# Kernel tuning notes

Measured on AMD Instinct MI355X. Metric: run time of the kernel, lower is better.

Reference implementation:

```python
import jax, jax.numpy as jnp
import numpy as np

D = 256   # hidden_dim
N = 1024  # total nodes
NP = 384  # paratope nodes
NE = 384  # epitope nodes
NC = 14   # atom channels


def setup_inputs() -> dict:
    key = jax.random.key(0)
    ks = jax.random.split(key, 24)
    s = 1.0 / np.sqrt(D)
    s3 = 1.0 / np.sqrt(3 * D)
    w = lambda k, shape, sc: (jax.random.normal(k, shape, jnp.float32) * sc)
    z = lambda: jnp.zeros((D,), jnp.float32)
    return {
        "H": w(ks[0], (N, D), 1.0),
        "X": w(ks[1], (N, NC, 3), 1.0),
        "paratope_mask": jnp.zeros((N,), bool).at[:NP].set(True),
        "epitope_mask": jnp.zeros((N,), bool).at[NP:NP + NE].set(True),
        "res_w1": w(ks[2], (1, D), 1.0), "res_b1": z(),
        "res_w2": w(ks[3], (D, D), s), "res_b2": z(),
        "atom_w1": w(ks[4], (1, D), 1.0), "atom_b1": z(),
        "atom_w2": w(ks[5], (D, D), s), "atom_b2": z(),
        "sim_weight": jnp.float32(0.5),
        "int_w1": w(ks[6], (3 * D, D), s3), "int_b1": z(),
        "int_w2": w(ks[7], (D, D), s), "int_b2": z(),
        "wl": w(ks[8], (D, D), s),
        "wr": w(ks[9], (D, D), s),
        "wg_w": w(ks[10], (D, D), s), "wg_b": z(),
        "wq_w": w(ks[11], (D, D), s), "wq_b": z(),
        "wk_w": w(ks[12], (D, D), s), "wk_b": z(),
        "wv_w": w(ks[13], (D, D), s), "wv_b": z(),
    }


def _mlp2(x, w1, b1, w2, b2):
    return jax.nn.silu(x @ w1 + b1) @ w2 + b2


def reference(H, X, paratope_mask, epitope_mask,
              res_w1, res_b1, res_w2, res_b2,
              atom_w1, atom_b1, atom_w2, atom_b2,
              sim_weight,
              int_w1, int_b1, int_w2, int_b2,
              wl, wr, wg_w, wg_b, wq_w, wq_b, wk_w, wk_b, wv_w, wv_b):
    p_idx = jnp.nonzero(paratope_mask, size=NP)[0]
    e_idx = jnp.nonzero(epitope_mask, size=NE)[0]
    Hp = H[p_idx]                      # [NP, D]
    He = H[e_idx]                      # [NE, D]
    Xp_ca = X[p_idx, 1]                # [NP, 3] (CA atom)
    Xe_ca = X[e_idx, 1]                # [NE, 3]

    dX = Xp_ca[:, None, :] - Xe_ca[None, :, :]         # [NP, NE, 3]
    S = jnp.sum(dX * dX, axis=-1, keepdims=True)       # [NP, NE, 1]
    # original computes S_residue and S_atom with identical formula
    S_res = _mlp2(S, res_w1, res_b1, res_w2, res_b2)
    S_atom = _mlp2(S, atom_w1, atom_b1, atom_w2, atom_b2)
    wmix = jax.nn.sigmoid(sim_weight)
    S_comb = wmix * S_res + (1.0 - wmix) * S_atom      # [NP, NE, D]

    Hp_e = jnp.broadcast_to(Hp[:, None, :], (NP, NE, D))
    He_e = jnp.broadcast_to(He[None, :, :], (NP, NE, D))
    Z_in = jnp.concatenate([Hp_e, He_e, S_comb], axis=-1)  # [NP, NE, 3D]
    Z = _mlp2(Z_in, int_w1, int_b1, int_w2, int_b2)        # [NP, NE, D]

    I = (Hp @ wl)[:, None, :] * (He @ wr)[None, :, :]      # outer-product interaction
    gate = jax.nn.sigmoid(Z @ wg_w + wg_b)
    f_tri = gate * I

    Q = Z @ wq_w + wq_b
    K = Z @ wk_w + wk_b
    V = Z @ wv_w + wv_b
    scores = jnp.einsum('ped,pfd->pef', Q, K) / (D ** 0.5)  # [NP, NE, NE]
    A = jax.nn.softmax(scores, axis=-1)
    f_att = jnp.einsum('pef,pfd->ped', A, V)

    H_tri = f_tri + f_att                                   # [NP, NE, D]
    return H.at[p_idx].set(H_tri.mean(axis=1))
```

## Files before the change

kernel.cpp:

```cpp
#include <hip/hip_runtime.h>

#define NPAR 384
#define NEPI 384
#define DD   256
#define NTAB 4096
#define SMAX 96.0f
#define SDELTA (SMAX / NTAB)
#define SINVD (NTAB / SMAX)

using bf16x8 = __bf16 __attribute__((ext_vector_type(8)));
using bf16x2 = __bf16 __attribute__((ext_vector_type(2)));
using f32x4  = float __attribute__((ext_vector_type(4)));

#if defined(__has_builtin)
#if __has_builtin(__builtin_amdgcn_cvt_pk_bf16_f32)
#define HAVE_PK_BF16 1
#endif
#endif

__device__ __forceinline__ float sigm(float x) { return 1.0f / (1.0f + __expf(-x)); }
__device__ __forceinline__ float silu(float x) { return x / (1.0f + __expf(-x)); }
__device__ __forceinline__ unsigned short f2bf(float f) {
  unsigned u = __float_as_uint(f);
  u += 0x7fffu + ((u >> 16) & 1u);
  return (unsigned short)(u >> 16);
}
__device__ __forceinline__ float bf2f(unsigned u16) {
  return __uint_as_float(u16 << 16);
}
__device__ __forceinline__ float bf2f_lo(unsigned w) {
  return __uint_as_float(w << 16);
}
__device__ __forceinline__ float bf2f_hi(unsigned w) {
  return __uint_as_float(w & 0xffff0000u);
}
__device__ __forceinline__ uint2 pack4(float a, float b, float c, float d) {
  uint2 r;
#ifdef HAVE_PK_BF16
  bf16x2 lo = __builtin_amdgcn_cvt_pk_bf16_f32(a, b);
  bf16x2 hi = __builtin_amdgcn_cvt_pk_bf16_f32(c, d);
  r.x = __builtin_bit_cast(unsigned, lo);
  r.y = __builtin_bit_cast(unsigned, hi);
#else
  r.x = (unsigned)f2bf(a) | ((unsigned)f2bf(b) << 16);
  r.y = (unsigned)f2bf(c) | ((unsigned)f2bf(d) << 16);
#endif
  return r;
}


__global__ void prep_kernel(
    const float* __restrict__ H, const float* __restrict__ wl,
    const float* __restrict__ wr, const float* __restrict__ int_w1,
    const float* __restrict__ res_w2, const float* __restrict__ atom_w2,
    const float* __restrict__ res_b2, const float* __restrict__ atom_b2,
    const float* __restrict__ int_b1, const float* __restrict__ simw,
    const float* __restrict__ wq_b, const float* __restrict__ wk_w,
    float* __restrict__ Hpl, float* __restrict__ Her,
    float* __restrict__ P1, float* __restrict__ P2,
    float* __restrict__ MrF, float* __restrict__ MaF,
    float* __restrict__ cvec, float* __restrict__ gv,
    float* __restrict__ wkT) {
  __shared__ float tile[32][33];
  const int b = blockIdx.x, t = threadIdx.x;
  if (b < 64) {
    const int bx = b & 7, by = b >> 3;
    const int tx = t & 31, ty = t >> 5;
    for (int r = 0; r < 32; r += 8)
      tile[ty + r][tx] = wk_w[(by * 32 + ty + r) * 256 + bx * 32 + tx];
    __syncthreads();
    for (int r = 0; r < 32; r += 8)
      wkT[(bx * 32 + ty + r) * 256 + by * 32 + tx] = tile[tx][ty + r];
  } else if (b < 576) {
    const int bb = b - 64;
    const int i = bb & 255;
    const bool isMa = bb >= 256;
    const float wmix = 1.0f / (1.0f + __expf(-simw[0]));
    const float sc = isMa ? (1.0f - wmix) : wmix;
    const float* W2 = isMa ? atom_w2 : res_w2;
    float acc = 0.f;
#pragma unroll 8
    for (int k = 0; k < 256; ++k)
      acc += W2[i * 256 + k] * int_w1[(512 + k) * 256 + t];
    (isMa ? MaF : MrF)[i * 256 + t] = acc * sc;
  } else if (b < 584) {
    const int bb = b - 576;
    const float wmix = 1.0f / (1.0f + __expf(-simw[0]));
    float acc = (bb == 0) ? int_b1[t] : 0.f;
#pragma unroll
    for (int k = bb * 32; k < bb * 32 + 32; ++k) {
      float bm = wmix * res_b2[k] + (1.0f - wmix) * atom_b2[k];
      acc += bm * int_w1[(512 + k) * 256 + t];
    }
    atomicAdd(&cvec[t], acc);
  } else if (b < 648) {
    const int lane = t & 63, w = t >> 6;
    const int d = (b - 584) * 4 + w;
    float acc = 0.f;
#pragma unroll
    for (int i = 0; i < 4; ++i) {
      const int c = i * 64 + lane;
      acc += wk_w[d * 256 + c] * wq_b[c];
    }
    acc += __shfl_xor(acc, 1);
    acc += __shfl_xor(acc, 2);
    acc += __shfl_xor(acc, 4);
    acc += __shfl_xor(acc, 8);
    acc += __shfl_xor(acc, 16);
    acc += __shfl_xor(acc, 32);
    if (lane == 0) gv[d] = acc;
  } else {
    const int idx = b - 648;
    const int seg = idx / 384, r = idx % 384;
    const float* A;
    const float* B;
    float* C;
    switch (seg) {
      case 0:  A = H + r * 256;            B = wl;              C = Hpl + r * 256; break;
      case 1:  A = H + (NPAR + r) * 256;   B = wr;              C = Her + r * 256; break;
      case 2:  A = H + r * 256;            B = int_w1;          C = P1 + r * 256;  break;
      default: A = H + (NPAR + r) * 256;   B = int_w1 + 65536;  C = P2 + r * 256;  break;
    }
    float acc = 0.f;
#pragma unroll 8
    for (int k = 0; k < 256; ++k)
      acc += A[k] * B[k * 256 + t];
    C[t] = acc;
  }
}

__global__ void mm_rows(const float* __restrict__ A, const float* __restrict__ B,
                        float* __restrict__ C) {
  const int r = blockIdx.x, j = threadIdx.x;
  float acc = 0.f;
#pragma unroll 8
  for (int k = 0; k < 256; ++k)
    acc += A[r * 256 + k] * B[k * 256 + j];
  C[r * 256 + j] = acc;
}

__global__ void pack_kernel(const float* __restrict__ MrF, const float* __restrict__ MaF,
                            const float* __restrict__ w2, const float* __restrict__ wg,
                            const float* __restrict__ WqkF, unsigned short* __restrict__ wpack) {
  const int idx = blockIdx.x * 256 + threadIdx.x;
  const int m = idx >> 16;
  const int r = idx & 65535;
  const int chunk = r >> 9;
  const int lane = (r >> 3) & 63;
  const int j = r & 7;
  const int k = (chunk >> 4) * 32 + (lane >> 4) * 8 + j;
  const int n = (chunk & 15) * 16 + (lane & 15);
  const float* src;
  switch (m) {
    case 0: src = MrF; break;
    case 1: src = MaF; break;
    case 2: src = w2; break;
    case 3: src = wg; break;
    default: src = WqkF; break;
  }
  wpack[idx] = f2bf(src[k * 256 + n]);
}


__device__ __forceinline__ void zero_acc4(f32x4 (&acc)[4][4]) {
#pragma unroll
  for (int mt = 0; mt < 4; ++mt)
#pragma unroll
    for (int nt = 0; nt < 4; ++nt)
      acc[mt][nt] = (f32x4){0.f, 0.f, 0.f, 0.f};
}

__device__ __forceinline__ void gemm4(f32x4 (&acc)[4][4],
                                      const unsigned short* __restrict__ wp,
                                      const unsigned short* ub, int lane, int wv) {
  const int l15 = lane & 15, l4 = lane >> 4;
#pragma unroll
  for (int ks = 0; ks < 8; ++ks) {
    bf16x8 a[4];
#pragma unroll
    for (int mt = 0; mt < 4; ++mt)
      a[mt] = *reinterpret_cast<const bf16x8*>(wp + ((ks * 16 + wv * 4 + mt) * 64 + lane) * 8);
#pragma unroll
    for (int nt = 0; nt < 4; ++nt) {
      bf16x8 b = *reinterpret_cast<const bf16x8*>(ub + (nt * 16 + l15) * 264 + ks * 32 + l4 * 8);
#pragma unroll
      for (int mt = 0; mt < 4; ++mt)
        acc[mt][nt] = __builtin_amdgcn_mfma_f32_16x16x32_bf16(a[mt], b, acc[mt][nt], 0, 0, 0);
    }
  }
}

__device__ __forceinline__ void fill_u(unsigned short* ub, const float* Sv,
                                       const float* __restrict__ w1,
                                       const float* __restrict__ b1, int t) {
  const int dg = t & 31, rb = t >> 5;
  const f32x4 w1a = *reinterpret_cast<const f32x4*>(&w1[dg * 8]);
  const f32x4 w1b = *reinterpret_cast<const f32x4*>(&w1[dg * 8 + 4]);
  const f32x4 b1a = *reinterpret_cast<const f32x4*>(&b1[dg * 8]);
  const f32x4 b1b = *reinterpret_cast<const f32x4*>(&b1[dg * 8 + 4]);
#pragma unroll
  for (int i = 0; i < 8; ++i) {
    const int e = rb + i * 8;
    const float s = Sv[e];
    uint2 lo = pack4(silu(fmaf(s, w1a[0], b1a[0])), silu(fmaf(s, w1a[1], b1a[1])),
                     silu(fmaf(s, w1a[2], b1a[2])), silu(fmaf(s, w1a[3], b1a[3])));
    uint2 hi = pack4(silu(fmaf(s, w1b[0], b1b[0])), silu(fmaf(s, w1b[1], b1b[1])),
                     silu(fmaf(s, w1b[2], b1b[2])), silu(fmaf(s, w1b[3], b1b[3])));
    uint4 pk = {lo.x, lo.y, hi.x, hi.y};
    *reinterpret_cast<uint4*>(&ub[e * 264 + dg * 8]) = pk;
  }
}


__global__ __launch_bounds__(256, 3) void tab_kernel(
    const float* __restrict__ res_w1, const float* __restrict__ res_b1,
    const float* __restrict__ atom_w1, const float* __restrict__ atom_b1,
    const unsigned short* __restrict__ wpack, unsigned short* __restrict__ tab) {
  __shared__ __align__(16) unsigned short ubuf[64 * 264];
  __shared__ float Sv[64];
  const int t = threadIdx.x, lane = t & 63, wv = t >> 6;
  const int l15 = lane & 15, l4 = lane >> 4;
  const int n0 = blockIdx.x * 64;
  if (t < 64) Sv[t] = (n0 + t) * SDELTA;
  __syncthreads();
  f32x4 acc[4][4];
  zero_acc4(acc);
  fill_u(ubuf, Sv, res_w1, res_b1, t);
  __syncthreads();
  gemm4(acc, wpack + 0 * 65536, ubuf, lane, wv);
  __syncthreads();
  fill_u(ubuf, Sv, atom_w1, atom_b1, t);
  __syncthreads();
  gemm4(acc, wpack + 1 * 65536, ubuf, lane, wv);
#pragma unroll
  for (int mt = 0; mt < 4; ++mt) {
    const int d = wv * 64 + mt * 16 + l4 * 4;
#pragma unroll
    for (int nt = 0; nt < 4; ++nt) {
      const int n = n0 + nt * 16 + l15;
      *reinterpret_cast<uint2*>(&tab[n * 256 + d]) =
          pack4(acc[mt][nt][0], acc[mt][nt][1], acc[mt][nt][2], acc[mt][nt][3]);
    }
  }
}


__global__ __launch_bounds__(256, 3) void pair_kernel(
    const float* __restrict__ Xg, const unsigned short* __restrict__ tab,
    const float* __restrict__ int_b2, const float* __restrict__ wg_b,
    const unsigned short* __restrict__ wpack, const float* __restrict__ cvec,
    const float* __restrict__ P1, const float* __restrict__ P2,
    const float* __restrict__ Hpl, const float* __restrict__ Her,
    float* __restrict__ ftri, unsigned short* __restrict__ Zsw) {
  __shared__ __align__(16) unsigned short ubuf[64 * 264];
  __shared__ float Sv[64];
  __shared__ float pc[DD];
  const int t = threadIdx.x, lane = t & 63, wv = t >> 6;
  const int l15 = lane & 15, l4 = lane >> 4;
  const int p = blockIdx.x / 6, cc = blockIdx.x % 6, e0 = cc * 64;
  const int d0 = wv * 64;

  if (t < 64) {
    const int e = e0 + t;
    float dx = Xg[p * 42 + 3] - Xg[(NPAR + e) * 42 + 3];
    float dy = Xg[p * 42 + 4] - Xg[(NPAR + e) * 42 + 4];
    float dz = Xg[p * 42 + 5] - Xg[(NPAR + e) * 42 + 5];
    Sv[t] = dx * dx + dy * dy + dz * dz;
  }
  pc[t] = P1[p * DD + t] + cvec[t];
  __syncthreads();

  {
    const int dg = t & 31, rb = t >> 5;
    const f32x4 pca = *reinterpret_cast<const f32x4*>(&pc[dg * 8]);
    const f32x4 pcb = *reinterpret_cast<const f32x4*>(&pc[dg * 8 + 4]);
#pragma unroll
    for (int i = 0; i < 8; ++i) {
      const int e = rb + i * 8;
      float sv = Sv[e] * SINVD;
      int idx = (int)sv;
      idx = idx > (NTAB - 2) ? (NTAB - 2) : idx;
      const float fr = sv - (float)idx;
      const uint4 t0 = *reinterpret_cast<const uint4*>(&tab[idx * 256 + dg * 8]);
      const uint4 t1 = *reinterpret_cast<const uint4*>(&tab[(idx + 1) * 256 + dg * 8]);
      const f32x4 p2a = *reinterpret_cast<const f32x4*>(&P2[(e0 + e) * DD + dg * 8]);
      const f32x4 p2b = *reinterpret_cast<const f32x4*>(&P2[(e0 + e) * DD + dg * 8 + 4]);
      float z0 = bf2f_lo(t0.x), z1 = bf2f_hi(t0.x), z2 = bf2f_lo(t0.y), z3 = bf2f_hi(t0.y);
      float z4 = bf2f_lo(t0.z), z5 = bf2f_hi(t0.z), z6 = bf2f_lo(t0.w), z7 = bf2f_hi(t0.w);
      z0 = fmaf(fr, bf2f_lo(t1.x) - z0, z0) + pca[0] + p2a[0];
      z1 = fmaf(fr, bf2f_hi(t1.x) - z1, z1) + pca[1] + p2a[1];
      z2 = fmaf(fr, bf2f_lo(t1.y) - z2, z2) + pca[2] + p2a[2];
      z3 = fmaf(fr, bf2f_hi(t1.y) - z3, z3) + pca[3] + p2a[3];
      z4 = fmaf(fr, bf2f_lo(t1.z) - z4, z4) + pcb[0] + p2b[0];
      z5 = fmaf(fr, bf2f_hi(t1.z) - z5, z5) + pcb[1] + p2b[1];
      z6 = fmaf(fr, bf2f_lo(t1.w) - z6, z6) + pcb[2] + p2b[2];
      z7 = fmaf(fr, bf2f_hi(t1.w) - z7, z7) + pcb[3] + p2b[3];
      uint2 lo = pack4(silu(z0), silu(z1), silu(z2), silu(z3));
      uint2 hi = pack4(silu(z4), silu(z5), silu(z6), silu(z7));
      uint4 pk = {lo.x, lo.y, hi.x, hi.y};
      *reinterpret_cast<uint4*>(&ubuf[e * 264 + dg * 8]) = pk;
    }
  }
  __syncthreads();

  f32x4 acc[4][4];
  zero_acc4(acc);
  gemm4(acc, wpack + 2 * 65536, ubuf, lane, wv);
  __syncthreads();
#pragma unroll
  for (int mt = 0; mt < 4; ++mt) {
    const int d = d0 + mt * 16 + l4 * 4;
    const f32x4 bb = *reinterpret_cast<const f32x4*>(&int_b2[d]);
#pragma unroll
    for (int nt = 0; nt < 4; ++nt) {
      const int e = nt * 16 + l15;
      *reinterpret_cast<uint2*>(&ubuf[e * 264 + d]) =
          pack4(acc[mt][nt][0] + bb[0], acc[mt][nt][1] + bb[1],
                acc[mt][nt][2] + bb[2], acc[mt][nt][3] + bb[3]);
    }
  }
  __syncthreads();

  {
    unsigned short* Zd = Zsw + (size_t)p * 98304 + (size_t)(cc * 4 + wv) * 4096 + lane * 8;
#pragma unroll
    for (int ks = 0; ks < 8; ++ks) {
      *reinterpret_cast<uint4*>(Zd + ks * 512) =
          *reinterpret_cast<const uint4*>(&ubuf[(wv * 16 + l15) * 264 + ks * 32 + l4 * 8]);
    }
  }

  zero_acc4(acc);
  gemm4(acc, wpack + 3 * 65536, ubuf, lane, wv);
#pragma unroll
  for (int mt = 0; mt < 4; ++mt) {
    const int d = d0 + mt * 16 + l4 * 4;
    const f32x4 bb = *reinterpret_cast<const f32x4*>(&wg_b[d]);
    const f32x4 hl = *reinterpret_cast<const f32x4*>(&Hpl[p * DD + d]);
    f32x4 fs = (f32x4){0.f, 0.f, 0.f, 0.f};
#pragma unroll
    for (int nt = 0; nt < 4; ++nt) {
      const int e = e0 + nt * 16 + l15;
      const f32x4 hr = *reinterpret_cast<const f32x4*>(&Her[e * DD + d]);
#pragma unroll
      for (int r = 0; r < 4; ++r)
        fs[r] += sigm(acc[mt][nt][r] + bb[r]) * hr[r];
    }
#pragma unroll
    for (int r = 0; r < 4; ++r) {
      float v = fs[r] * hl[r];
      v += __shfl_xor(v, 1);
      v += __shfl_xor(v, 2);
      v += __shfl_xor(v, 4);
      v += __shfl_xor(v, 8);
      if (l15 == 0) atomicAdd(&ftri[p * DD + d + r], v);
    }
  }
}


__global__ __launch_bounds__(256, 3) void attn_kernel(
    const unsigned short* __restrict__ Zsw, const float* __restrict__ gv,
    const unsigned short* __restrict__ wpack, float* __restrict__ cbufg) {
  __shared__ __align__(16) unsigned short Tc[64 * 264];
  __shared__ float red[256];
  __shared__ float red2[256];
  const int t = threadIdx.x, lane = t & 63, wv = t >> 6;
  const int l15 = lane & 15, l4 = lane >> 4;
  const int xcd = blockIdx.x & 7, inner = blockIdx.x >> 3;
  const int p = (inner / 6) * 8 + xcd, c = inner % 6;
  const unsigned short* Zsp = Zsw + (size_t)p * 98304;
  const unsigned short* wqk = wpack + 4 * 65536;

  {
    f32x4 ta[4][4];
    zero_acc4(ta);
    const unsigned short* Tb = Zsp + (size_t)(c * 4) * 4096 + lane * 8;
    bf16x8 bcur[4], bnxt[4];
#pragma unroll
    for (int nt = 0; nt < 4; ++nt)
      bcur[nt] = *reinterpret_cast<const bf16x8*>(Tb + nt * 4096);
#pragma unroll
    for (int ks = 0; ks < 8; ++ks) {
      if (ks < 7) {
#pragma unroll
        for (int nt = 0; nt < 4; ++nt)
          bnxt[nt] = *reinterpret_cast<const bf16x8*>(Tb + nt * 4096 + (ks + 1) * 512);
      }
      bf16x8 a[4];
#pragma unroll
      for (int mt = 0; mt < 4; ++mt)
        a[mt] = *reinterpret_cast<const bf16x8*>(wqk + ((ks * 16 + wv * 4 + mt) * 64 + lane) * 8);
#pragma unroll
      for (int nt = 0; nt < 4; ++nt)
#pragma unroll
        for (int mt = 0; mt < 4; ++mt)
          ta[mt][nt] = __builtin_amdgcn_mfma_f32_16x16x32_bf16(a[mt], bcur[nt], ta[mt][nt], 0, 0, 0);
      if (ks < 7) {
#pragma unroll
        for (int nt = 0; nt < 4; ++nt) bcur[nt] = bnxt[nt];
      }
    }
#pragma unroll
    for (int mt = 0; mt < 4; ++mt) {
      const int d = wv * 64 + mt * 16 + l4 * 4;
      const f32x4 gq = *reinterpret_cast<const f32x4*>(&gv[d]);
#pragma unroll
      for (int nt = 0; nt < 4; ++nt) {
        const int e = nt * 16 + l15;
        *reinterpret_cast<uint2*>(&Tc[e * 264 + d]) =
            pack4((ta[mt][nt][0] + gq[0]) * 0.0625f, (ta[mt][nt][1] + gq[1]) * 0.0625f,
                  (ta[mt][nt][2] + gq[2]) * 0.0625f, (ta[mt][nt][3] + gq[3]) * 0.0625f);
      }
    }
  }
  __syncthreads();

  f32x4 sc[4][6];
#pragma unroll
  for (int mt = 0; mt < 4; ++mt)
#pragma unroll
    for (int s = 0; s < 6; ++s) sc[mt][s] = (f32x4){0.f, 0.f, 0.f, 0.f};

  {
    const unsigned short* Sb = Zsp + (size_t)wv * 4096 + lane * 8;
    bf16x8 bcur[6], bnxt[6];
#pragma unroll
    for (int s = 0; s < 6; ++s)
      bcur[s] = *reinterpret_cast<const bf16x8*>(Sb + s * 16384);
#pragma unroll
    for (int ks = 0; ks < 8; ++ks) {
      if (ks < 7) {
#pragma unroll
        for (int s = 0; s < 6; ++s)
          bnxt[s] = *reinterpret_cast<const bf16x8*>(Sb + s * 16384 + (ks + 1) * 512);
      }
      bf16x8 a[4];
#pragma unroll
      for (int mt = 0; mt < 4; ++mt)
        a[mt] = *reinterpret_cast<const bf16x8*>(&Tc[(mt * 16 + l15) * 264 + ks * 32 + l4 * 8]);
#pragma unroll
      for (int s = 0; s < 6; ++s)
#pragma unroll
        for (int mt = 0; mt < 4; ++mt)
          sc[mt][s] = __builtin_amdgcn_mfma_f32_16x16x32_bf16(a[mt], bcur[s], sc[mt][s], 0, 0, 0);
      if (ks < 7) {
#pragma unroll
        for (int s = 0; s < 6; ++s) bcur[s] = bnxt[s];
      }
    }
  }

  float rmax[4][4];
#pragma unroll
  for (int mt = 0; mt < 4; ++mt) {
#pragma unroll
    for (int r = 0; r < 4; ++r) {
      float m = -1e30f;
#pragma unroll
      for (int s = 0; s < 6; ++s) m = fmaxf(m, sc[mt][s][r]);
      m = fmaxf(m, __shfl_xor(m, 1));
      m = fmaxf(m, __shfl_xor(m, 2));
      m = fmaxf(m, __shfl_xor(m, 4));
      m = fmaxf(m, __shfl_xor(m, 8));
      rmax[mt][r] = m;
    }
  }
  if (l15 == 0) {
#pragma unroll
    for (int mt = 0; mt < 4; ++mt)
#pragma unroll
      for (int r = 0; r < 4; ++r)
        red[wv * 64 + mt * 16 + l4 * 4 + r] = rmax[mt][r];
  }
  __syncthreads();
#pragma unroll
  for (int mt = 0; mt < 4; ++mt) {
#pragma unroll
    for (int r = 0; r < 4; ++r) {
      const int row = mt * 16 + l4 * 4 + r;
      rmax[mt][r] = fmaxf(fmaxf(red[row], red[64 + row]), fmaxf(red[128 + row], red[192 + row]));
    }
  }

  float rsum[4][4];
#pragma unroll
  for (int mt = 0; mt < 4; ++mt) {
#pragma unroll
    for (int r = 0; r < 4; ++r) {
      float sSum = 0.f;
#pragma unroll
      for (int s = 0; s < 6; ++s) {
        float e = __expf(sc[mt][s][r] - rmax[mt][r]);
        sc[mt][s][r] = e;
        sSum += e;
      }
      sSum += __shfl_xor(sSum, 1);
      sSum += __shfl_xor(sSum, 2);
      sSum += __shfl_xor(sSum, 4);
      sSum += __shfl_xor(sSum, 8);
      rsum[mt][r] = sSum;
    }
  }
  if (l15 == 0) {
#pragma unroll
    for (int mt = 0; mt < 4; ++mt)
#pragma unroll
      for (int r = 0; r < 4; ++r)
        red2[wv * 64 + mt * 16 + l4 * 4 + r] = rsum[mt][r];
  }
  __syncthreads();
  float rinv[4][4];
#pragma unroll
  for (int mt = 0; mt < 4; ++mt) {
#pragma unroll
    for (int r = 0; r < 4; ++r) {
      const int row = mt * 16 + l4 * 4 + r;
      rinv[mt][r] = 1.0f / (red2[row] + red2[64 + row] + red2[128 + row] + red2[192 + row]);
    }
  }

#pragma unroll
  for (int s = 0; s < 6; ++s) {
    float v = 0.f;
#pragma unroll
    for (int mt = 0; mt < 4; ++mt)
#pragma unroll
      for (int r = 0; r < 4; ++r)
        v += sc[mt][s][r] * rinv[mt][r];
    v += __shfl_xor(v, 16);
    v += __shfl_xor(v, 32);
    if (lane < 16)
      atomicAdd(&cbufg[p * NEPI + s * 64 + wv * 16 + lane], v);
  }
}


__global__ __launch_bounds__(256) void out_kernel(
    const unsigned short* __restrict__ Zsw, const float* __restrict__ ftri,
    const float* __restrict__ cbufg, const float* __restrict__ wvw,
    const float* __restrict__ wvb, float* __restrict__ out) {
  __shared__ float cb[NEPI];
  __shared__ float part[16][257];
  __shared__ float u[DD];
  const int p = blockIdx.x, t = threadIdx.x;
  const int lane = t & 63, wv = t >> 6;
  const int l15 = lane & 15, l4 = lane >> 4;
  for (int i = t; i < NEPI; i += 256) cb[i] = cbufg[p * NEPI + i];
  __syncthreads();
  const unsigned short* Zsp = Zsw + (size_t)p * 98304;
  float a16[16];
#pragma unroll
  for (int j = 0; j < 16; ++j) a16[j] = 0.f;
#pragma unroll 4
  for (int grp = 0; grp < 24; ++grp) {
    const float w = cb[grp * 16 + l15];
    const uint4 z0 = *reinterpret_cast<const uint4*>(Zsp + grp * 4096 + wv * 512 + lane * 8);
    const uint4 z1 = *reinterpret_cast<const uint4*>(Zsp + grp * 4096 + (wv + 4) * 512 + lane * 8);
    a16[0] = fmaf(w, bf2f(z0.x & 0xffffu), a16[0]);
    a16[1] = fmaf(w, bf2f(z0.x >> 16), a16[1]);
    a16[2] = fmaf(w, bf2f(z0.y & 0xffffu), a16[2]);
    a16[3] = fmaf(w, bf2f(z0.y >> 16), a16[3]);
    a16[4] = fmaf(w, bf2f(z0.z & 0xffffu), a16[4]);
    a16[5] = fmaf(w, bf2f(z0.z >> 16), a16[5]);
    a16[6] = fmaf(w, bf2f(z0.w & 0xffffu), a16[6]);
    a16[7] = fmaf(w, bf2f(z0.w >> 16), a16[7]);
    a16[8]  = fmaf(w, bf2f(z1.x & 0xffffu), a16[8]);
    a16[9]  = fmaf(w, bf2f(z1.x >> 16), a16[9]);
    a16[10] = fmaf(w, bf2f(z1.y & 0xffffu), a16[10]);
    a16[11] = fmaf(w, bf2f(z1.y >> 16), a16[11]);
    a16[12] = fmaf(w, bf2f(z1.z & 0xffffu), a16[12]);
    a16[13] = fmaf(w, bf2f(z1.z >> 16), a16[13]);
    a16[14] = fmaf(w, bf2f(z1.w & 0xffffu), a16[14]);
    a16[15] = fmaf(w, bf2f(z1.w >> 16), a16[15]);
  }
#pragma unroll
  for (int j = 0; j < 8; ++j) part[l15][wv * 32 + l4 * 8 + j] = a16[j];
#pragma unroll
  for (int j = 0; j < 8; ++j) part[l15][128 + wv * 32 + l4 * 8 + j] = a16[8 + j];
  __syncthreads();
  float uu = 0.f;
#pragma unroll
  for (int g = 0; g < 16; ++g) uu += part[g][t];
  u[t] = uu;
  __syncthreads();
  float acc = ftri[p * DD + t] + 384.0f * wvb[t];
#pragma unroll 8
  for (int d = 0; d < DD; ++d)
    acc = fmaf(u[d], wvw[d * DD + t], acc);
  out[p * DD + t] = acc * (1.0f / 384.0f);
}


extern "C" void kernel_launch(void* const* d_in, const int* in_sizes, int n_in,
                              void* d_out, int out_size, void* d_ws, size_t ws_size,
                              hipStream_t stream) {
  (void)in_sizes; (void)n_in; (void)out_size; (void)ws_size;
  const float* H = (const float*)d_in[0];
  const float* X = (const float*)d_in[1];
  const float* res_w1 = (const float*)d_in[4];
  const float* res_b1 = (const float*)d_in[5];
  const float* res_w2 = (const float*)d_in[6];
  const float* res_b2 = (const float*)d_in[7];
  const float* atom_w1 = (const float*)d_in[8];
  const float* atom_b1 = (const float*)d_in[9];
  const float* atom_w2 = (const float*)d_in[10];
  const float* atom_b2 = (const float*)d_in[11];
  const float* simw = (const float*)d_in[12];
  const float* int_w1 = (const float*)d_in[13];
  const float* int_b1 = (const float*)d_in[14];
  const float* int_w2 = (const float*)d_in[15];
  const float* int_b2 = (const float*)d_in[16];
  const float* wl = (const float*)d_in[17];
  const float* wr = (const float*)d_in[18];
  const float* wg_w = (const float*)d_in[19];
  const float* wg_b = (const float*)d_in[20];
  const float* wq_w = (const float*)d_in[21];
  const float* wq_b = (const float*)d_in[22];
  const float* wk_w = (const float*)d_in[23];
  const float* wv_w = (const float*)d_in[25];
  const float* wv_b = (const float*)d_in[26];

  char* ws = (char*)d_ws;
  unsigned short* wpack = (unsigned short*)(ws + 0);
  float* MrF   = (float*)(ws + 655360);
  float* MaF   = (float*)(ws + 917504);
  float* WqkF  = (float*)(ws + 1179648);
  float* wkT   = (float*)(ws + 1441792);
  float* cvec  = (float*)(ws + 1703936);
  float* gv    = (float*)(ws + 1704960);
  float* P1    = (float*)(ws + 1705984);
  float* P2    = (float*)(ws + 2099200);
  float* Hpl   = (float*)(ws + 2492416);
  float* Her   = (float*)(ws + 2885632);
  float* ftri  = (float*)(ws + 3278848);
  float* cbufg = (float*)(ws + 3672064);
  unsigned short* Zsw = (unsigned short*)(ws + 4261888);
  unsigned short* tab = (unsigned short*)(ws + 79759360);

  hipMemsetAsync(ftri, 0, 393216 + 589824, stream);
  hipMemsetAsync(cvec, 0, DD * sizeof(float), stream);
  prep_kernel<<<2184, 256, 0, stream>>>(H, wl, wr, int_w1, res_w2, atom_w2,
                                        res_b2, atom_b2, int_b1, simw, wq_b, wk_w,
                                        Hpl, Her, P1, P2, MrF, MaF, cvec, gv, wkT);
  mm_rows<<<256, 256, 0, stream>>>(wq_w, wkT, WqkF);
  pack_kernel<<<1280, 256, 0, stream>>>(MrF, MaF, int_w2, wg_w, WqkF, wpack);
  tab_kernel<<<NTAB / 64, 256, 0, stream>>>(res_w1, res_b1, atom_w1, atom_b1, wpack, tab);
  pair_kernel<<<2304, 256, 0, stream>>>(X, tab, int_b2, wg_b, wpack, cvec,
                                        P1, P2, Hpl, Her, ftri, Zsw);
  attn_kernel<<<2304, 256, 0, stream>>>(Zsw, gv, wpack, cbufg);
  out_kernel<<<384, 256, 0, stream>>>(Zsw, ftri, cbufg, wv_w, wv_b, (float*)d_out);
  hipMemcpyAsync((float*)d_out + NPAR * DD, H + NPAR * DD,
                 (1024 - NPAR) * DD * sizeof(float), hipMemcpyDeviceToDevice, stream);
}
```

Measured before the change: 344.5 us.

## Fold Wq·WkT into prep kernel and split output reduction across more blocks

The separate wk transpose and mm_rows launch are removed. The Wq·Wk^T product is now computed inside prep_kernel by reading wk rows directly with vector loads. The cvec bias reduction becomes a single block, which drops one memset and the atomics. The output kernel is split into outa_kernel, which spreads each paratope's weighted Z reduction over three blocks and combines them with atomics into ubufg, and out2_kernel, which applies wv; this raises parallelism over the 75MB Z read at the cost of one extra launch.

Measured after the change: 343.2 us. Within noise of the previous version (-0.4%).

```diff
diff --git a/kernel.cpp b/kernel.cpp
--- a/kernel.cpp
+++ b/kernel.cpp
@@ -56,25 +56,17 @@
     const float* __restrict__ res_b2, const float* __restrict__ atom_b2,
     const float* __restrict__ int_b1, const float* __restrict__ simw,
     const float* __restrict__ wq_b, const float* __restrict__ wk_w,
+    const float* __restrict__ wq_w,
     float* __restrict__ Hpl, float* __restrict__ Her,
     float* __restrict__ P1, float* __restrict__ P2,
     float* __restrict__ MrF, float* __restrict__ MaF,
     float* __restrict__ cvec, float* __restrict__ gv,
-    float* __restrict__ wkT) {
-  __shared__ float tile[32][33];
+    float* __restrict__ WqkF) {
+  __shared__ float sbuf[256];
   const int b = blockIdx.x, t = threadIdx.x;
-  if (b < 64) {
-    const int bx = b & 7, by = b >> 3;
-    const int tx = t & 31, ty = t >> 5;
-    for (int r = 0; r < 32; r += 8)
-      tile[ty + r][tx] = wk_w[(by * 32 + ty + r) * 256 + bx * 32 + tx];
-    __syncthreads();
-    for (int r = 0; r < 32; r += 8)
-      wkT[(bx * 32 + ty + r) * 256 + by * 32 + tx] = tile[tx][ty + r];
-  } else if (b < 576) {
-    const int bb = b - 64;
-    const int i = bb & 255;
-    const bool isMa = bb >= 256;
+  if (b < 512) {
+    const int i = b & 255;
+    const bool isMa = b >= 256;
     const float wmix = 1.0f / (1.0f + __expf(-simw[0]));
     const float sc = isMa ? (1.0f - wmix) : wmix;
     const float* W2 = isMa ? atom_w2 : res_w2;
@@ -83,19 +75,18 @@
     for (int k = 0; k < 256; ++k)
       acc += W2[i * 256 + k] * int_w1[(512 + k) * 256 + t];
     (isMa ? MaF : MrF)[i * 256 + t] = acc * sc;
-  } else if (b < 584) {
-    const int bb = b - 576;
+  } else if (b == 512) {
     const float wmix = 1.0f / (1.0f + __expf(-simw[0]));
-    float acc = (bb == 0) ? int_b1[t] : 0.f;
-#pragma unroll
-    for (int k = bb * 32; k < bb * 32 + 32; ++k) {
+    float acc = int_b1[t];
+#pragma unroll 8
+    for (int k = 0; k < 256; ++k) {
       float bm = wmix * res_b2[k] + (1.0f - wmix) * atom_b2[k];
       acc += bm * int_w1[(512 + k) * 256 + t];
     }
-    atomicAdd(&cvec[t], acc);
-  } else if (b < 648) {
+    cvec[t] = acc;
+  } else if (b < 577) {
     const int lane = t & 63, w = t >> 6;
-    const int d = (b - 584) * 4 + w;
+    const int d = (b - 513) * 4 + w;
     float acc = 0.f;
 #pragma unroll
     for (int i = 0; i < 4; ++i) {
@@ -109,8 +100,23 @@
     acc += __shfl_xor(acc, 16);
     acc += __shfl_xor(acc, 32);
     if (lane == 0) gv[d] = acc;
+  } else if (b < 833) {
+    const int r = b - 577;
+    sbuf[t] = wq_w[r * 256 + t];
+    __syncthreads();
+    const float* wkrow = wk_w + t * 256;
+    float a0 = 0.f, a1 = 0.f, a2 = 0.f, a3 = 0.f;
+#pragma unroll 4
+    for (int k = 0; k < 256; k += 4) {
+      const f32x4 wv4 = *reinterpret_cast<const f32x4*>(&wkrow[k]);
+      a0 = fmaf(sbuf[k + 0], wv4[0], a0);
+      a1 = fmaf(sbuf[k + 1], wv4[1], a1);
+      a2 = fmaf(sbuf[k + 2], wv4[2], a2);
+      a3 = fmaf(sbuf[k + 3], wv4[3], a3);
+    }
+    WqkF[r * 256 + t] = (a0 + a1) + (a2 + a3);
   } else {
-    const int idx = b - 648;
+    const int idx = b - 833;
     const int seg = idx / 384, r = idx % 384;
     const float* A;
     const float* B;
@@ -127,16 +133,6 @@
       acc += A[k] * B[k * 256 + t];
     C[t] = acc;
   }
-}
-
-__global__ void mm_rows(const float* __restrict__ A, const float* __restrict__ B,
-                        float* __restrict__ C) {
-  const int r = blockIdx.x, j = threadIdx.x;
-  float acc = 0.f;
-#pragma unroll 8
-  for (int k = 0; k < 256; ++k)
-    acc += A[r * 256 + k] * B[k * 256 + j];
-  C[r * 256 + j] = acc;
 }
 
 __global__ void pack_kernel(const float* __restrict__ MrF, const float* __restrict__ MaF,
@@ -536,25 +532,25 @@
 }
 
 
-__global__ __launch_bounds__(256) void out_kernel(
-    const unsigned short* __restrict__ Zsw, const float* __restrict__ ftri,
-    const float* __restrict__ cbufg, const float* __restrict__ wvw,
-    const float* __restrict__ wvb, float* __restrict__ out) {
-  __shared__ float cb[NEPI];
+__global__ __launch_bounds__(256) void outa_kernel(
+    const unsigned short* __restrict__ Zsw, const float* __restrict__ cbufg,
+    float* __restrict__ ubufg) {
+  __shared__ float cb[128];
   __shared__ float part[16][257];
-  __shared__ float u[DD];
-  const int p = blockIdx.x, t = threadIdx.x;
+  const int p = blockIdx.x / 3, th = blockIdx.x % 3, g0 = th * 8;
+  const int t = threadIdx.x;
   const int lane = t & 63, wv = t >> 6;
   const int l15 = lane & 15, l4 = lane >> 4;
-  for (int i = t; i < NEPI; i += 256) cb[i] = cbufg[p * NEPI + i];
+  if (t < 128) cb[t] = cbufg[p * NEPI + g0 * 16 + t];
   __syncthreads();
   const unsigned short* Zsp = Zsw + (size_t)p * 98304;
   float a16[16];
 #pragma unroll
   for (int j = 0; j < 16; ++j) a16[j] = 0.f;
-#pragma unroll 4
-  for (int grp = 0; grp < 24; ++grp) {
-    const float w = cb[grp * 16 + l15];
+#pragma unroll
+  for (int gr = 0; gr < 8; ++gr) {
+    const int grp = g0 + gr;
+    const float w = cb[gr * 16 + l15];
     const uint4 z0 = *reinterpret_cast<const uint4*>(Zsp + grp * 4096 + wv * 512 + lane * 8);
     const uint4 z1 = *reinterpret_cast<const uint4*>(Zsp + grp * 4096 + (wv + 4) * 512 + lane * 8);
     a16[0] = fmaf(w, bf2f(z0.x & 0xffffu), a16[0]);
@@ -582,7 +578,17 @@
   float uu = 0.f;
 #pragma unroll
   for (int g = 0; g < 16; ++g) uu += part[g][t];
-  u[t] = uu;
+  atomicAdd(&ubufg[p * DD + t], uu);
+}
+
+
+__global__ __launch_bounds__(256) void out2_kernel(
+    const float* __restrict__ ubufg, const float* __restrict__ ftri,
+    const float* __restrict__ wvw, const float* __restrict__ wvb,
+    float* __restrict__ out) {
+  __shared__ float u[DD];
+  const int p = blockIdx.x, t = threadIdx.x;
+  u[t] = ubufg[p * DD + t];
   __syncthreads();
   float acc = ftri[p * DD + t] + 384.0f * wvb[t];
 #pragma unroll 8
@@ -626,30 +632,29 @@
   float* MrF   = (float*)(ws + 655360);
   float* MaF   = (float*)(ws + 917504);
   float* WqkF  = (float*)(ws + 1179648);
-  float* wkT   = (float*)(ws + 1441792);
-  float* cvec  = (float*)(ws + 1703936);
-  float* gv    = (float*)(ws + 1704960);
-  float* P1    = (float*)(ws + 1705984);
-  float* P2    = (float*)(ws + 2099200);
-  float* Hpl   = (float*)(ws + 2492416);
-  float* Her   = (float*)(ws + 2885632);
-  float* ftri  = (float*)(ws + 3278848);
-  float* cbufg = (float*)(ws + 3672064);
-  unsigned short* Zsw = (unsigned short*)(ws + 4261888);
-  unsigned short* tab = (unsigned short*)(ws + 79759360);
-
-  hipMemsetAsync(ftri, 0, 393216 + 589824, stream);
-  hipMemsetAsync(cvec, 0, DD * sizeof(float), stream);
-  prep_kernel<<<2184, 256, 0, stream>>>(H, wl, wr, int_w1, res_w2, atom_w2,
-                                        res_b2, atom_b2, int_b1, simw, wq_b, wk_w,
-                                        Hpl, Her, P1, P2, MrF, MaF, cvec, gv, wkT);
-  mm_rows<<<256, 256, 0, stream>>>(wq_w, wkT, WqkF);
+  float* cvec  = (float*)(ws + 1441792);
+  float* gv    = (float*)(ws + 1442816);
+  float* P1    = (float*)(ws + 1443840);
+  float* P2    = (float*)(ws + 1837056);
+  float* Hpl   = (float*)(ws + 2230272);
+  float* Her   = (float*)(ws + 2623488);
+  float* ftri  = (float*)(ws + 3016704);
+  float* cbufg = (float*)(ws + 3409920);
+  float* ubufg = (float*)(ws + 3999744);
+  unsigned short* Zsw = (unsigned short*)(ws + 4392960);
+  unsigned short* tab = (unsigned short*)(ws + 79890432);
+
+  hipMemsetAsync(ftri, 0, 393216 + 589824 + 393216, stream);
+  prep_kernel<<<2369, 256, 0, stream>>>(H, wl, wr, int_w1, res_w2, atom_w2,
+                                        res_b2, atom_b2, int_b1, simw, wq_b, wk_w, wq_w,
+                                        Hpl, Her, P1, P2, MrF, MaF, cvec, gv, WqkF);
   pack_kernel<<<1280, 256, 0, stream>>>(MrF, MaF, int_w2, wg_w, WqkF, wpack);
   tab_kernel<<<NTAB / 64, 256, 0, stream>>>(res_w1, res_b1, atom_w1, atom_b1, wpack, tab);
   pair_kernel<<<2304, 256, 0, stream>>>(X, tab, int_b2, wg_b, wpack, cvec,
                                         P1, P2, Hpl, Her, ftri, Zsw);
   attn_kernel<<<2304, 256, 0, stream>>>(Zsw, gv, wpack, cbufg);
-  out_kernel<<<384, 256, 0, stream>>>(Zsw, ftri, cbufg, wv_w, wv_b, (float*)d_out);
+  outa_kernel<<<1152, 256, 0, stream>>>(Zsw, cbufg, ubufg);
+  out2_kernel<<<384, 256, 0, stream>>>(ubufg, ftri, wv_w, wv_b, (float*)d_out);
   hipMemcpyAsync((float*)d_out + NPAR * DD, H + NPAR * DD,
                  (1024 - NPAR) * DD * sizeof(float), hipMemcpyDeviceToDevice, stream);
 }
```
